# Optimization experiments

Measured on AMD Instinct MI355X. Metric: run time of the kernel, lower is better.

The kernel has to match this reference:

```python
import jax, jax.numpy as jnp
import numpy as np

N = 20000      # nodes per snapshot
E = 160000     # edges per snapshot
T = 8          # timesteps
F_IN = 256     # nfeat
HEADS = 4      # GAT heads
C = 128        # nhid_graph (per-head GAT out, concat=False -> mean)
GH = 128       # nhid_gru
NC = 2         # nclass
NEG_SLOPE = 0.2


def setup_inputs() -> dict:
    key = jax.random.key(0)
    ks = jax.random.split(key, 16)
    s = 0.05
    return {
        "graph": jax.random.randint(ks[0], (T, 2, E), 0, N),
        "fts": jax.random.normal(ks[1], (T, N, F_IN), dtype=jnp.float32),
        "time_steps": T,
        # GATConv params (PyG-style): lin weight, att_src/att_dst, bias
        "W_gat": jax.random.normal(ks[2], (F_IN, HEADS * C), dtype=jnp.float32) * s,
        "att_src": jax.random.normal(ks[3], (HEADS, C), dtype=jnp.float32) * s,
        "att_dst": jax.random.normal(ks[4], (HEADS, C), dtype=jnp.float32) * s,
        "b_gat": jax.random.normal(ks[5], (C,), dtype=jnp.float32) * s,
        # GRU params (torch layout: [3H, in], gates order r,z,n)
        "W_ih": jax.random.normal(ks[6], (3 * GH, C), dtype=jnp.float32) * s,
        "W_hh": jax.random.normal(ks[7], (3 * GH, GH), dtype=jnp.float32) * s,
        "b_ih": jax.random.normal(ks[8], (3 * GH,), dtype=jnp.float32) * s,
        "b_hh": jax.random.normal(ks[9], (3 * GH,), dtype=jnp.float32) * s,
        # Attention ('general'): linear_in [H,H] no bias, linear_out [H,2H] no bias
        "W_att_in": jax.random.normal(ks[10], (GH, GH), dtype=jnp.float32) * s,
        "W_att_out": jax.random.normal(ks[11], (GH, 2 * GH), dtype=jnp.float32) * s,
        # final classifier
        "W_cls": jax.random.normal(ks[12], (NC, GH), dtype=jnp.float32) * s,
        "b_cls": jax.random.normal(ks[13], (NC,), dtype=jnp.float32) * s,
    }


def _segment_softmax(logits, seg, num_segments):
    # logits: [E', H], seg: [E'] destination node ids
    m = jax.ops.segment_max(logits, seg, num_segments=num_segments)
    m = jnp.where(jnp.isfinite(m), m, 0.0)
    e = jnp.exp(logits - m[seg])
    s = jax.ops.segment_sum(e, seg, num_segments=num_segments)
    return e / (s[seg] + 1e-16)


def _gat_step(x, edge_index, W_gat, att_src, att_dst, b_gat):
    # PyG GATConv: concat=False (mean over heads), negative_slope=0.2,
    # add_self_loops=True; eval mode so attention dropout is identity.
    n = x.shape[0]
    xw = (x @ W_gat).reshape(n, HEADS, C)                 # [N,H,C]
    loops = jnp.arange(n, dtype=edge_index.dtype)
    src = jnp.concatenate([edge_index[0], loops])         # [E']
    dst = jnp.concatenate([edge_index[1], loops])
    a_src = jnp.einsum('nhc,hc->nh', xw, att_src)         # [N,H]
    a_dst = jnp.einsum('nhc,hc->nh', xw, att_dst)
    alpha = jax.nn.leaky_relu(a_src[src] + a_dst[dst], NEG_SLOPE)  # [E',H]
    alpha = _segment_softmax(alpha, dst, n)
    msg = xw[src] * alpha[..., None]                      # [E',H,C]
    out = jax.ops.segment_sum(msg, dst, num_segments=n)   # [N,H,C]
    return out.mean(axis=1) + b_gat                       # [N,C]


def _gru(y, W_ih, W_hh, b_ih, b_hh):
    # y: [T, N, C]; torch GRU equations, h0 = 0
    n = y.shape[1]
    def step(h, x):
        gi = x @ W_ih.T + b_ih
        gh = h @ W_hh.T + b_hh
        i_r, i_z, i_n = jnp.split(gi, 3, axis=-1)
        h_r, h_z, h_n = jnp.split(gh, 3, axis=-1)
        r = jax.nn.sigmoid(i_r + h_r)
        z = jax.nn.sigmoid(i_z + h_z)
        nn_ = jnp.tanh(i_n + r * h_n)
        h_new = (1.0 - z) * nn_ + z * h
        return h_new, h_new
    h0 = jnp.zeros((n, GH), dtype=y.dtype)
    last, full = jax.lax.scan(step, h0, y)
    return full, last  # [T,N,GH], [N,GH]


def reference(graph, fts, time_steps, W_gat, att_src, att_dst, b_gat,
              W_ih, W_hh, b_ih, b_hh, W_att_in, W_att_out, W_cls, b_cls):
    # per-timestep GAT + leaky_relu(0.2)
    ys = [jax.nn.leaky_relu(
            _gat_step(fts[i], graph[i], W_gat, att_src, att_dst, b_gat),
            NEG_SLOPE)
          for i in range(time_steps)]
    y = jnp.stack(ys)                                     # [T,N,C]
    context, last = _gru(y, W_ih, W_hh, b_ih, b_hh)
    query = last[:, None, :]                              # [N,1,GH]
    context = jnp.transpose(context, (1, 0, 2))           # [N,T,GH]
    # Attention('general')
    q = query @ W_att_in.T                                # [N,1,GH]
    scores = jnp.einsum('nod,ntd->not', q, context)       # [N,1,T]
    w = jax.nn.softmax(scores, axis=-1)
    mix = jnp.einsum('not,ntd->nod', w, context)          # [N,1,GH]
    combined = jnp.concatenate([mix, q], axis=-1)         # [N,1,2GH]
    att_out = jnp.tanh(combined @ W_att_out.T)            # [N,1,GH]
    output = jax.nn.leaky_relu(att_out.reshape(-1, GH), NEG_SLOPE)
    logits = output @ W_cls.T + b_cls                     # [N,NC]
    return jax.nn.log_softmax(logits, axis=1)
```

## Files before the change

### kernel.cpp

```cpp
#include <hip/hip_runtime.h>
#include <hip/hip_bf16.h>
#include <math.h>

#define N_NODES 20000
#define N_EDGES 160000
#define T_STEPS 8
#define F_INC   256
#define HEADS   4
#define CCH     128
#define KC      512
#define GHD     128
#define G3      384
#define SLOPE   0.2f
#define SEG     (N_EDGES + N_NODES)

typedef unsigned short u16;
typedef __attribute__((ext_vector_type(8))) short bf16x8;
typedef __attribute__((ext_vector_type(4))) float f32x4;

__device__ __forceinline__ float leakyf(float x) { return x > 0.f ? x : SLOPE * x; }
__device__ __forceinline__ float b2f(u16 u) {
  union { unsigned int i; float f; } x; x.i = ((unsigned int)u) << 16; return x.f;
}
__device__ __forceinline__ u16 f2b(float f) {
  union { float f; unsigned int i; } u; u.f = f;
  unsigned int r = u.i + 0x7FFFu + ((u.i >> 16) & 1u);
  return (u16)(r >> 16);
}
__device__ __forceinline__ float sigf(float x) { return 1.f / (1.f + expf(-x)); }

__device__ __forceinline__ void gload16(const void* g, void* l) {
  __builtin_amdgcn_global_load_lds(
      (const __attribute__((address_space(1))) unsigned int*)g,
      (__attribute__((address_space(3))) unsigned int*)l, 16, 0, 0);
}

template <int OBF, int FUSE>
__global__ __launch_bounds__(256) void gemm_bf16(
    const u16* __restrict__ A, const u16* __restrict__ B,
    const float* __restrict__ bias, void* __restrict__ Cout,
    int M, int K, int Nt, int swz,
    const float* __restrict__ attS, const float* __restrict__ attD,
    float* __restrict__ asrc, float* __restrict__ adst)
{
  __shared__ u16 As[128][32];
  __shared__ u16 Bs[128][32];
  __shared__ float s_as[128], s_ad[128];
  const int tid  = threadIdx.x;
  const int wave = tid >> 6, lane = tid & 63;
  const int wr = (wave >> 1) * 64, wc = (wave & 1) * 64;
  int bx = blockIdx.x, by = blockIdx.y;
  if (swz) {
    const int gx = gridDim.x;
    const int nwg = gx * (int)gridDim.y;
    const int lin = by * gx + bx;
    const int q = nwg >> 3, r = nwg & 7;
    const int xcd = lin & 7, idx = lin >> 3;
    const int wg = (xcd < r ? xcd * (q + 1) : r * (q + 1) + (xcd - r) * q) + idx;
    bx = wg % gx; by = wg / gx;
  }
  const int bm = by * 128, bn = bx * 128;
  const int l15 = lane & 15, g = lane >> 4;

  if (FUSE && tid < 128) { s_as[tid] = 0.f; s_ad[tid] = 0.f; }

  const int sr = tid >> 2, sd = tid & 3;
  const int ss = sd ^ ((sr >> 1) & 3);
  const u16* aS0 = A + (size_t)min(bm + sr,      M - 1) * K + ss * 8;
  const u16* aS1 = A + (size_t)min(bm + 64 + sr, M - 1) * K + ss * 8;
  const u16* bS0 = B + (size_t)(bn + sr)      * K + ss * 8;
  const u16* bS1 = B + (size_t)(bn + 64 + sr) * K + ss * 8;
  u16* lA0 = &As[0][0] + (size_t)(tid & ~63) * 8;
  u16* lA1 = lA0 + 2048;
  u16* lB0 = &Bs[0][0] + (size_t)(tid & ~63) * 8;
  u16* lB1 = lB0 + 2048;

  f32x4 acc[4][4];
  #pragma unroll
  for (int m = 0; m < 4; ++m)
    #pragma unroll
    for (int n = 0; n < 4; ++n)
      #pragma unroll
      for (int j = 0; j < 4; ++j) acc[m][n][j] = 0.f;

  const int nK = K >> 5;
  for (int kt = 0; kt < nK; ++kt) {
    const int ko = kt * 32;
    gload16(aS0 + ko, lA0);
    gload16(aS1 + ko, lA1);
    gload16(bS0 + ko, lB0);
    gload16(bS1 + ko, lB1);
    __syncthreads();
    bf16x8 af[4], bfr[4];
    #pragma unroll
    for (int m = 0; m < 4; ++m) {
      int row = wr + m * 16 + l15;
      af[m] = *(const bf16x8*)&As[row][(g ^ ((row >> 1) & 3)) * 8];
      int rowb = wc + m * 16 + l15;
      bfr[m] = *(const bf16x8*)&Bs[rowb][(g ^ ((rowb >> 1) & 3)) * 8];
    }
    #pragma unroll
    for (int m = 0; m < 4; ++m)
      #pragma unroll
      for (int n = 0; n < 4; ++n)
        acc[m][n] = __builtin_amdgcn_mfma_f32_16x16x32_bf16(af[m], bfr[n], acc[m][n], 0, 0, 0);
    __syncthreads();
  }
  #pragma unroll
  for (int m = 0; m < 4; ++m) {
    int row0 = bm + wr + m * 16 + g * 4;
    #pragma unroll
    for (int n = 0; n < 4; ++n) {
      int col = bn + wc + n * 16 + l15;
      float bv = bias ? bias[col] : 0.f;
      #pragma unroll
      for (int j = 0; j < 4; ++j) {
        int row = row0 + j;
        if (row < M) {
          float v = acc[m][n][j] + bv;
          if (OBF) ((u16*)Cout)[(size_t)row * Nt + col] = f2b(v);
          else     ((float*)Cout)[(size_t)row * Nt + col] = v;
        }
      }
    }
  }
  if (FUSE) {
    float ps[4][4], pd[4][4];
    #pragma unroll
    for (int m = 0; m < 4; ++m)
      #pragma unroll
      for (int j = 0; j < 4; ++j) { ps[m][j] = 0.f; pd[m][j] = 0.f; }
    #pragma unroll
    for (int n = 0; n < 4; ++n) {
      int cl = wc + n * 16 + l15;
      float wsv = attS[bn + cl], wdv = attD[bn + cl];
      #pragma unroll
      for (int m = 0; m < 4; ++m)
        #pragma unroll
        for (int j = 0; j < 4; ++j) {
          ps[m][j] = fmaf(acc[m][n][j], wsv, ps[m][j]);
          pd[m][j] = fmaf(acc[m][n][j], wdv, pd[m][j]);
        }
    }
    #pragma unroll
    for (int m = 0; m < 4; ++m)
      #pragma unroll
      for (int j = 0; j < 4; ++j)
        #pragma unroll
        for (int msk = 8; msk >= 1; msk >>= 1) {
          ps[m][j] += __shfl_xor(ps[m][j], msk);
          pd[m][j] += __shfl_xor(pd[m][j], msk);
        }
    if (l15 == 0) {
      #pragma unroll
      for (int m = 0; m < 4; ++m)
        #pragma unroll
        for (int j = 0; j < 4; ++j) {
          atomicAdd(&s_as[wr + m * 16 + g * 4 + j], ps[m][j]);
          atomicAdd(&s_ad[wr + m * 16 + g * 4 + j], pd[m][j]);
        }
    }
    __syncthreads();
    if (tid < 128) {
      int row = bm + tid;
      if (row < M) {
        int h = bn >> 7;
        asrc[(size_t)row * 4 + h] = s_as[tid];
        adst[(size_t)row * 4 + h] = s_ad[tid];
      }
    }
  }
}

__global__ void convert_f32_bf16(const float* __restrict__ src, u16* __restrict__ dst, int n) {
  int i = (blockIdx.x * 256 + threadIdx.x) * 8;
  if (i >= n) return;
  float4 v0 = *(const float4*)(src + i);
  float4 v1 = *(const float4*)(src + i + 4);
  bf16x8 o;
  o[0] = (short)f2b(v0.x); o[1] = (short)f2b(v0.y);
  o[2] = (short)f2b(v0.z); o[3] = (short)f2b(v0.w);
  o[4] = (short)f2b(v1.x); o[5] = (short)f2b(v1.y);
  o[6] = (short)f2b(v1.z); o[7] = (short)f2b(v1.w);
  *(bf16x8*)(dst + i) = o;
}

__global__ void convert_weights(const float* __restrict__ w_ih, const float* __restrict__ w_hh,
                                const float* __restrict__ w_in, const float* __restrict__ w_out,
                                u16* __restrict__ wihb, u16* __restrict__ whhb,
                                u16* __restrict__ winb, u16* __restrict__ woutb)
{
  int i = blockIdx.x * 256 + threadIdx.x;
  const float* src; u16* dst; int base;
  if      (i < 6144)  { src = w_ih;  dst = wihb;  base = i; }
  else if (i < 12288) { src = w_hh;  dst = whhb;  base = i - 6144; }
  else if (i < 14336) { src = w_in;  dst = winb;  base = i - 12288; }
  else                { src = w_out; dst = woutb; base = i - 14336; }
  int o = base * 8;
  float4 v0 = *(const float4*)(src + o);
  float4 v1 = *(const float4*)(src + o + 4);
  bf16x8 ov;
  ov[0] = (short)f2b(v0.x); ov[1] = (short)f2b(v0.y);
  ov[2] = (short)f2b(v0.z); ov[3] = (short)f2b(v0.w);
  ov[4] = (short)f2b(v1.x); ov[5] = (short)f2b(v1.y);
  ov[6] = (short)f2b(v1.z); ov[7] = (short)f2b(v1.w);
  *(bf16x8*)(dst + o) = ov;
}

__global__ void conv_transpose_wgat(const float* __restrict__ src, u16* __restrict__ dst) {
  int idx = blockIdx.x * 256 + threadIdx.x;
  if (idx >= KC * F_INC) return;
  int n = idx >> 8, k = idx & 255;
  dst[(size_t)n * F_INC + k] = f2b(src[(size_t)k * KC + n]);
}

__global__ void count_kernel(const int* __restrict__ graph, int* __restrict__ counts) {
  int e = blockIdx.x * 256 + threadIdx.x;
  int t = blockIdx.y;
  if (e < N_EDGES) {
    int d = graph[(size_t)t * 2 * N_EDGES + N_EDGES + e];
    atomicAdd(&counts[t * N_NODES + d], 1);
  }
}

__global__ __launch_bounds__(1024) void scan_kernel(
    const int* __restrict__ counts, int* __restrict__ offs)
{
  const int t = blockIdx.x;
  const int tid = threadIdx.x, lane = tid & 63, w = tid >> 6;
  __shared__ int s_wt[16];
  int carry = 0;
  const int base_abs = t * SEG;
  for (int base = 0; base < N_NODES; base += 1024) {
    int i = base + tid;
    int v = (i < N_NODES) ? (counts[t * N_NODES + i] + 1) : 0;
    int x = v;
    #pragma unroll
    for (int d = 1; d < 64; d <<= 1) {
      int nvl = __shfl_up(x, d, 64);
      if (lane >= d) x += nvl;
    }
    if (lane == 63) s_wt[w] = x;
    __syncthreads();
    if (tid < 16) {
      int y = s_wt[tid];
      #pragma unroll
      for (int d = 1; d < 16; d <<= 1) {
        int nvl = __shfl_up(y, d, 64);
        if (tid >= d) y += nvl;
      }
      s_wt[tid] = y;
    }
    __syncthreads();
    int wbase = (w > 0) ? s_wt[w - 1] : 0;
    int total = s_wt[15];
    if (i < N_NODES) offs[t * (N_NODES + 1) + i] = base_abs + carry + wbase + x - v;
    carry += total;
    __syncthreads();
  }
  if (tid == 0) offs[t * (N_NODES + 1) + N_NODES] = base_abs + carry;
}

__global__ void scatter_kernel(const int* __restrict__ graph, const int* __restrict__ offs,
                               int* __restrict__ cursor, int* __restrict__ ssrc)
{
  int i = blockIdx.x * 256 + threadIdx.x;
  int t = blockIdx.y;
  if (i >= SEG) return;
  int s, d;
  if (i < N_EDGES) {
    s = graph[(size_t)t * 2 * N_EDGES + i];
    d = graph[(size_t)t * 2 * N_EDGES + N_EDGES + i];
  } else {
    s = d = i - N_EDGES;
  }
  int pos = offs[t * (N_NODES + 1) + d] + atomicAdd(&cursor[t * N_NODES + d], 1);
  ssrc[pos] = s;
}

__global__ __launch_bounds__(256) void aggregate_kernel(
    const u16* __restrict__ xw, const float* __restrict__ a_src,
    const float* __restrict__ a_dst, const float* __restrict__ b_gat,
    const int* __restrict__ offs, const int* __restrict__ ssrc,
    u16* __restrict__ yout)
{
  const int wv = threadIdx.x >> 6, lane = threadIdx.x & 63;
  const int nd = blockIdx.x * 4 + wv;
  const int t  = blockIdx.y;
  __shared__ float s_w[4][64][4];
  __shared__ int   s_s[4][64];
  const int ob = t * (N_NODES + 1) + nd;
  const int beg = offs[ob], end = offs[ob + 1];
  const size_t rowbase = (size_t)t * N_NODES;
  const float4 adv = *(const float4*)&a_dst[(rowbase + nd) * 4];
  const int hl = lane >> 4;

  float m0=-INFINITY, m1=-INFINITY, m2=-INFINITY, m3=-INFINITY;
  float s0=0.f, s1=0.f, s2=0.f, s3=0.f;
  float acc[8] = {0.f,0.f,0.f,0.f,0.f,0.f,0.f,0.f};

  for (int base = beg; base < end; base += 64) {
    int e = base + lane;
    float a0=-INFINITY, a1=-INFINITY, a2=-INFINITY, a3=-INFINITY;
    if (e < end) {
      int s = ssrc[e];
      s_s[wv][lane] = s;
      float4 av = *(const float4*)&a_src[(rowbase + s) * 4];
      a0 = leakyf(av.x + adv.x); a1 = leakyf(av.y + adv.y);
      a2 = leakyf(av.z + adv.z); a3 = leakyf(av.w + adv.w);
    }
    float c0m=a0, c1m=a1, c2m=a2, c3m=a3;
    #pragma unroll
    for (int msk = 32; msk >= 1; msk >>= 1) {
      c0m = fmaxf(c0m, __shfl_xor(c0m, msk)); c1m = fmaxf(c1m, __shfl_xor(c1m, msk));
      c2m = fmaxf(c2m, __shfl_xor(c2m, msk)); c3m = fmaxf(c3m, __shfl_xor(c3m, msk));
    }
    float n0 = fmaxf(m0, c0m), n1 = fmaxf(m1, c1m), n2 = fmaxf(m2, c2m), n3 = fmaxf(m3, c3m);
    float sc0 = expf(m0 - n0), sc1 = expf(m1 - n1), sc2 = expf(m2 - n2), sc3 = expf(m3 - n3);
    float sch = (hl == 0) ? sc0 : (hl == 1) ? sc1 : (hl == 2) ? sc2 : sc3;
    #pragma unroll
    for (int k = 0; k < 8; ++k) acc[k] *= sch;
    float w0 = expf(a0 - n0), w1 = expf(a1 - n1), w2 = expf(a2 - n2), w3 = expf(a3 - n3);
    s_w[wv][lane][0] = w0; s_w[wv][lane][1] = w1;
    s_w[wv][lane][2] = w2; s_w[wv][lane][3] = w3;
    float t0=w0, t1=w1, t2=w2, t3=w3;
    #pragma unroll
    for (int msk = 32; msk >= 1; msk >>= 1) {
      t0 += __shfl_xor(t0, msk); t1 += __shfl_xor(t1, msk);
      t2 += __shfl_xor(t2, msk); t3 += __shfl_xor(t3, msk);
    }
    s0 = s0 * sc0 + t0; s1 = s1 * sc1 + t1;
    s2 = s2 * sc2 + t2; s3 = s3 * sc3 + t3;
    m0 = n0; m1 = n1; m2 = n2; m3 = n3;

    const int cnt = min(64, end - base);
#define LDX(j) (*(const int4*)&xw[(rowbase + s_s[wv][(j)]) * KC + lane * 8])
#define FMA8(W, X)                                                        \
    { float _w = (W);                                                     \
      acc[0] = fmaf(_w, __uint_as_float((unsigned)(X).x << 16), acc[0]);  \
      acc[1] = fmaf(_w, __uint_as_float((unsigned)(X).x & 0xffff0000u), acc[1]); \
      acc[2] = fmaf(_w, __uint_as_float((unsigned)(X).y << 16), acc[2]);  \
      acc[3] = fmaf(_w, __uint_as_float((unsigned)(X).y & 0xffff0000u), acc[3]); \
      acc[4] = fmaf(_w, __uint_as_float((unsigned)(X).z << 16), acc[4]);  \
      acc[5] = fmaf(_w, __uint_as_float((unsigned)(X).z & 0xffff0000u), acc[5]); \
      acc[6] = fmaf(_w, __uint_as_float((unsigned)(X).w << 16), acc[6]);  \
      acc[7] = fmaf(_w, __uint_as_float((unsigned)(X).w & 0xffff0000u), acc[7]); }
    int4 g0 = {0,0,0,0}, g1 = {0,0,0,0}, g2 = {0,0,0,0}, g3 = {0,0,0,0};
    if (0 < cnt) g0 = LDX(0);
    if (1 < cnt) g1 = LDX(1);
    if (2 < cnt) g2 = LDX(2);
    if (3 < cnt) g3 = LDX(3);
    for (int b4 = 0; b4 < cnt; b4 += 4) {
      int4 p0 = {0,0,0,0}, p1 = {0,0,0,0}, p2 = {0,0,0,0}, p3 = {0,0,0,0};
      if (b4 + 4 < cnt) p0 = LDX(b4 + 4);
      if (b4 + 5 < cnt) p1 = LDX(b4 + 5);
      if (b4 + 6 < cnt) p2 = LDX(b4 + 6);
      if (b4 + 7 < cnt) p3 = LDX(b4 + 7);
      {                      FMA8(s_w[wv][b4 + 0][hl], g0); }
      if (b4 + 1 < cnt)      { FMA8(s_w[wv][b4 + 1][hl], g1); }
      if (b4 + 2 < cnt)      { FMA8(s_w[wv][b4 + 2][hl], g2); }
      if (b4 + 3 < cnt)      { FMA8(s_w[wv][b4 + 3][hl], g3); }
      g0 = p0; g1 = p1; g2 = p2; g3 = p3;
    }
#undef LDX
#undef FMA8
  }
  float sh = (hl == 0) ? s0 : (hl == 1) ? s1 : (hl == 2) ? s2 : s3;
  float inv = 1.f / (sh + 1e-16f);
  #pragma unroll
  for (int k = 0; k < 8; ++k) {
    acc[k] *= inv;
    acc[k] += __shfl_xor(acc[k], 16);
    acc[k] += __shfl_xor(acc[k], 32);
  }
  if (lane < 16) {
    bf16x8 ov;
    #pragma unroll
    for (int k = 0; k < 8; ++k) {
      float v = acc[k] * 0.25f + b_gat[lane * 8 + k];
      ov[k] = (short)f2b(leakyf(v));
    }
    *(bf16x8*)&yout[(rowbase + nd) * GHD + lane * 8] = ov;
  }
}

__global__ void gru_combine0(const u16* __restrict__ gi_t, const float* __restrict__ b_hh,
                             u16* __restrict__ ctx0, float* __restrict__ hf)
{
  int idx = blockIdx.x * 256 + threadIdx.x;
  if (idx >= N_NODES * GHD) return;
  int n = idx >> 7, c = idx & 127;
  size_t gb = (size_t)n * G3;
  float ir = b2f(gi_t[gb + c]), iz = b2f(gi_t[gb + 128 + c]), in_ = b2f(gi_t[gb + 256 + c]);
  float r = sigf(ir + b_hh[c]);
  float z = sigf(iz + b_hh[128 + c]);
  float nn = tanhf(in_ + r * b_hh[256 + c]);
  float h = (1.f - z) * nn;
  ctx0[idx] = f2b(h);
  hf[idx] = h;
}

__global__ __launch_bounds__(256) void gru_fused(
    const u16* __restrict__ hprev, const u16* __restrict__ Whh,
    const float* __restrict__ b_hh, const u16* __restrict__ gi_t,
    float* __restrict__ hf, u16* __restrict__ ctx_out)
{
  __shared__ u16 lds[64 * 384];
  u16 (*As)[32] = (u16(*)[32])lds;
  u16 (*Bs)[32] = (u16(*)[32])(lds + 64 * 32);
  const int tid = threadIdx.x, lane = tid & 63, wv = tid >> 6;
  const int l15 = lane & 15, g = lane >> 4;
  const int bm = blockIdx.x * 64;

  const int sr = tid >> 2, sd = tid & 3;
  const int ss = sd ^ ((sr >> 1) & 3);
  const u16* aS = hprev + (size_t)min(bm + sr, N_NODES - 1) * GHD + ss * 8;
  u16* lA = lds + (size_t)(tid & ~63) * 8;
  const u16* bS[6]; u16* lB[6];
  #pragma unroll
  for (int p = 0; p < 6; ++p) {
    int r = sr + p * 64;
    bS[p] = Whh + (size_t)r * GHD + ss * 8;
    lB[p] = lds + 64 * 32 + (size_t)(p * 256 + (tid & ~63)) * 8;
  }

  f32x4 acc[4][6];
  #pragma unroll
  for (int m = 0; m < 4; ++m)
    #pragma unroll
    for (int n = 0; n < 6; ++n)
      #pragma unroll
      for (int j = 0; j < 4; ++j) acc[m][n][j] = 0.f;

  #pragma unroll
  for (int kt = 0; kt < 4; ++kt) {
    const int ko = kt * 32;
    gload16(aS + ko, lA);
    #pragma unroll
    for (int p = 0; p < 6; ++p) gload16(bS[p] + ko, lB[p]);
    __syncthreads();
    bf16x8 af[4], bfr[6];
    #pragma unroll
    for (int m = 0; m < 4; ++m) {
      int row = m * 16 + l15;
      af[m] = *(const bf16x8*)&As[row][(g ^ ((row >> 1) & 3)) * 8];
    }
    #pragma unroll
    for (int n = 0; n < 6; ++n) {
      int row = wv * 96 + n * 16 + l15;
      bfr[n] = *(const bf16x8*)&Bs[row][(g ^ ((row >> 1) & 3)) * 8];
    }
    #pragma unroll
    for (int m = 0; m < 4; ++m)
      #pragma unroll
      for (int n = 0; n < 6; ++n)
        acc[m][n] = __builtin_amdgcn_mfma_f32_16x16x32_bf16(af[m], bfr[n], acc[m][n], 0, 0, 0);
    __syncthreads();
  }
  #pragma unroll
  for (int m = 0; m < 4; ++m)
    #pragma unroll
    for (int n = 0; n < 6; ++n) {
      int c = wv * 96 + n * 16 + l15;
      float bb = b_hh[c];
      #pragma unroll
      for (int j = 0; j < 4; ++j) {
        int r = m * 16 + g * 4 + j;
        lds[r * 384 + (((c >> 3) ^ (r & 7)) << 3) + (c & 7)] = f2b(acc[m][n][j] + bb);
      }
    }
  __syncthreads();
  {
    int r = tid >> 2, gr = bm + r;
    if (gr < N_NODES) {
      const int cg = (tid & 3) * 32;
      const size_t gb = (size_t)gr * G3;
      const size_t cb = (size_t)gr * GHD;
      #pragma unroll
      for (int q = 0; q < 4; ++q) {
        int c0 = cg + q * 8;
        int sl0 = ((c0 >> 3) ^ (r & 7));
        int sl1 = (((128 + c0) >> 3) ^ (r & 7));
        int sl2 = (((256 + c0) >> 3) ^ (r & 7));
        bf16x8 hr8 = *(bf16x8*)&lds[r * 384 + sl0 * 8];
        bf16x8 hz8 = *(bf16x8*)&lds[r * 384 + sl1 * 8];
        bf16x8 hn8 = *(bf16x8*)&lds[r * 384 + sl2 * 8];
        bf16x8 ir8 = *(const bf16x8*)&gi_t[gb + c0];
        bf16x8 iz8 = *(const bf16x8*)&gi_t[gb + 128 + c0];
        bf16x8 in8 = *(const bf16x8*)&gi_t[gb + 256 + c0];
        float4 hp0 = *(const float4*)&hf[cb + c0];
        float4 hp1 = *(const float4*)&hf[cb + c0 + 4];
        float hp[8] = {hp0.x, hp0.y, hp0.z, hp0.w, hp1.x, hp1.y, hp1.z, hp1.w};
        float cv[8];
        bf16x8 hv;
        #pragma unroll
        for (int k = 0; k < 8; ++k) {
          float rr = sigf(b2f((u16)ir8[k]) + b2f((u16)hr8[k]));
          float zz = sigf(b2f((u16)iz8[k]) + b2f((u16)hz8[k]));
          float nn = tanhf(b2f((u16)in8[k]) + rr * b2f((u16)hn8[k]));
          float h = (1.f - zz) * nn + zz * hp[k];
          cv[k] = h;
          hv[k] = (short)f2b(h);
        }
        *(float4*)&hf[cb + c0]     = make_float4(cv[0], cv[1], cv[2], cv[3]);
        *(float4*)&hf[cb + c0 + 4] = make_float4(cv[4], cv[5], cv[6], cv[7]);
        *(bf16x8*)&ctx_out[cb + c0] = hv;
      }
    }
  }
}

__global__ __launch_bounds__(256) void attn_mid(
    const u16* __restrict__ ctx, const float* __restrict__ q,
    u16* __restrict__ comb)
{
  const int node = blockIdx.x * 4 + (threadIdx.x >> 6);
  const int lane = threadIdx.x & 63;
  if (node >= N_NODES) return;
  const float q0 = q[(size_t)node * GHD + lane];
  const float q1 = q[(size_t)node * GHD + 64 + lane];
  float c0[T_STEPS], c1[T_STEPS], w[T_STEPS];
  float mx = -1e30f;
  #pragma unroll
  for (int t = 0; t < T_STEPS; ++t) {
    const u16* cr = ctx + ((size_t)t * N_NODES + node) * GHD;
    c0[t] = b2f(cr[lane]); c1[t] = b2f(cr[64 + lane]);
    float p = q0 * c0[t] + q1 * c1[t];
    #pragma unroll
    for (int m = 32; m >= 1; m >>= 1) p += __shfl_xor(p, m);
    w[t] = p;
    mx = fmaxf(mx, p);
  }
  float s = 0.f;
  #pragma unroll
  for (int t = 0; t < T_STEPS; ++t) { w[t] = expf(w[t] - mx); s += w[t]; }
  const float inv = 1.f / s;
  float m0 = 0.f, m1 = 0.f;
  #pragma unroll
  for (int t = 0; t < T_STEPS; ++t) { m0 = fmaf(w[t], c0[t], m0); m1 = fmaf(w[t], c1[t], m1); }
  m0 *= inv; m1 *= inv;
  u16* cb = comb + (size_t)node * 2 * GHD;
  cb[lane]       = f2b(m0);
  cb[64 + lane]  = f2b(m1);
  cb[128 + lane] = f2b(q0);
  cb[192 + lane] = f2b(q1);
}

__global__ __launch_bounds__(256) void logits_kernel(
    const u16* __restrict__ ao, const float* __restrict__ W_cls,
    const float* __restrict__ b_cls, float* __restrict__ out)
{
  const int node = blockIdx.x * 4 + (threadIdx.x >> 6);
  const int lane = threadIdx.x & 63;
  if (node >= N_NODES) return;
  float o0 = leakyf(tanhf(b2f(ao[(size_t)node * GHD + lane])));
  float o1 = leakyf(tanhf(b2f(ao[(size_t)node * GHD + 64 + lane])));
  float p0 = o0 * W_cls[lane] + o1 * W_cls[64 + lane];
  float p1 = o0 * W_cls[128 + lane] + o1 * W_cls[192 + lane];
  #pragma unroll
  for (int m = 32; m >= 1; m >>= 1) { p0 += __shfl_xor(p0, m); p1 += __shfl_xor(p1, m); }
  if (lane == 0) {
    float l0 = p0 + b_cls[0];
    float l1 = p1 + b_cls[1];
    float mx = fmaxf(l0, l1);
    float lse = mx + logf(expf(l0 - mx) + expf(l1 - mx));
    out[(size_t)node * 2 + 0] = l0 - lse;
    out[(size_t)node * 2 + 1] = l1 - lse;
  }
}

extern "C" void kernel_launch(void* const* d_in, const int* in_sizes, int n_in,
                              void* d_out, int out_size, void* d_ws, size_t ws_size,
                              hipStream_t stream)
{
  const int*   graph     = (const int*)  d_in[0];
  const float* fts       = (const float*)d_in[1];
  const float* W_gat     = (const float*)d_in[3];
  const float* att_src   = (const float*)d_in[4];
  const float* att_dst   = (const float*)d_in[5];
  const float* b_gat     = (const float*)d_in[6];
  const float* W_ih      = (const float*)d_in[7];
  const float* W_hh      = (const float*)d_in[8];
  const float* b_ih      = (const float*)d_in[9];
  const float* b_hh      = (const float*)d_in[10];
  const float* W_att_in  = (const float*)d_in[11];
  const float* W_att_out = (const float*)d_in[12];
  const float* W_cls     = (const float*)d_in[13];
  const float* b_cls     = (const float*)d_in[14];
  float* out = (float*)d_out;

  char* ws = (char*)d_ws;
  size_t off = 0;
  auto alloc = [&](size_t bytes) {
    void* p = ws + off;
    off = (off + bytes + 255) & ~(size_t)255;
    return p;
  };
  const size_t NT = (size_t)T_STEPS * N_NODES;
  u16*   wgatT = (u16*)alloc((size_t)KC * F_INC * 2);
  u16*   wihb  = (u16*)alloc((size_t)G3 * GHD * 2);
  u16*   whhb  = (u16*)alloc((size_t)G3 * GHD * 2);
  u16*   winb  = (u16*)alloc((size_t)GHD * GHD * 2);
  u16*   woutb = (u16*)alloc((size_t)GHD * 2 * GHD * 2);
  u16*   fbf   = (u16*)alloc(NT * F_INC * 2);
  u16*   xw    = (u16*)alloc(NT * KC * 2);
  float* asrc  = (float*)alloc(NT * 4 * 4);
  float* adst  = (float*)alloc(NT * 4 * 4);
  u16*   yall  = (u16*)alloc(NT * GHD * 2);
  u16*   giall = (u16*)alloc(NT * G3 * 2);
  u16*   ctx   = (u16*)alloc(NT * GHD * 2);
  float* hf    = (float*)alloc((size_t)N_NODES * GHD * 4);
  float* qf    = (float*)alloc((size_t)N_NODES * GHD * 4);
  u16*   comb  = (u16*)alloc((size_t)N_NODES * 2 * GHD * 2);
  u16*   aob   = (u16*)alloc((size_t)N_NODES * GHD * 2);
  int* counts  = (int*)alloc((size_t)2 * T_STEPS * N_NODES * 4);
  int* cursor  = counts + T_STEPS * N_NODES;
  int* offs    = (int*)alloc((size_t)T_STEPS * (N_NODES + 1) * 4);
  int* ssrc    = (int*)alloc((size_t)T_STEPS * SEG * 4);

  conv_transpose_wgat<<<dim3((KC * F_INC + 255) / 256), 256, 0, stream>>>(W_gat, wgatT);
  convert_weights<<<dim3(72), 256, 0, stream>>>(W_ih, W_hh, W_att_in, W_att_out,
                                                wihb, whhb, winb, woutb);

  hipMemsetAsync(counts, 0, (size_t)2 * T_STEPS * N_NODES * 4, stream);
  count_kernel<<<dim3(N_EDGES / 256, T_STEPS), 256, 0, stream>>>(graph, counts);
  scan_kernel<<<dim3(T_STEPS), 1024, 0, stream>>>(counts, offs);
  scatter_kernel<<<dim3((SEG + 255) / 256, T_STEPS), 256, 0, stream>>>(graph, offs, cursor, ssrc);

  convert_f32_bf16<<<dim3((int)(NT * F_INC / 8 / 256)), 256, 0, stream>>>(
      fts, fbf, (int)(NT * F_INC));

  gemm_bf16<1, 1><<<dim3(KC / 128, (int)(NT / 128)), 256, 0, stream>>>(
      fbf, wgatT, nullptr, xw, (int)NT, F_INC, KC, 1, att_src, att_dst, asrc, adst);

  aggregate_kernel<<<dim3(N_NODES / 4, T_STEPS), 256, 0, stream>>>(
      xw, asrc, adst, b_gat, offs, ssrc, yall);

  gemm_bf16<1, 0><<<dim3(G3 / 128, (int)(NT / 128)), 256, 0, stream>>>(
      yall, wihb, b_ih, giall, (int)NT, GHD, G3, 1, nullptr, nullptr, nullptr, nullptr);

  gru_combine0<<<dim3(N_NODES * GHD / 256), 256, 0, stream>>>(giall, b_hh, ctx, hf);
  for (int t = 1; t < T_STEPS; ++t) {
    gru_fused<<<dim3((N_NODES + 63) / 64), 256, 0, stream>>>(
        ctx + (size_t)(t - 1) * N_NODES * GHD, whhb, b_hh,
        giall + (size_t)t * N_NODES * G3, hf,
        ctx + (size_t)t * N_NODES * GHD);
  }

  gemm_bf16<0, 0><<<dim3(1, (N_NODES + 127) / 128), 256, 0, stream>>>(
      ctx + (size_t)(T_STEPS - 1) * N_NODES * GHD, winb, nullptr, qf,
      N_NODES, GHD, GHD, 0, nullptr, nullptr, nullptr, nullptr);
  attn_mid<<<dim3(N_NODES / 4), 256, 0, stream>>>(ctx, qf, comb);
  gemm_bf16<1, 0><<<dim3(1, (N_NODES + 127) / 128), 256, 0, stream>>>(
      comb, woutb, nullptr, aob, N_NODES, 2 * GHD, GHD, 0, nullptr, nullptr, nullptr, nullptr);
  logits_kernel<<<dim3(N_NODES / 4), 256, 0, stream>>>(aob, W_cls, b_cls, out);
}
```

Baseline: 870.6 us.

## Restructure GAT aggregation to 16-edge chunks with lane-per-(edge,head) softmax via shuffles

The aggregate kernel now handles edges in chunks of 16, with each lane owning one (edge, head) pair. It replaces the 64-edge chunks that needed four-head reductions per lane over six shuffle stages. Source indices and attention weights move between lanes with shuffles instead of shared memory, which removes LDS traffic. Padded edges get zero weight, and the gather loop issues eight row loads at a time. With about 9 edges per node, the aim is to cut wasted lanes and reduction work, at the cost of more shuffles per edge.

```diff
diff --git a/kernel.cpp b/kernel.cpp
--- a/kernel.cpp
+++ b/kernel.cpp
@@ -287,54 +287,17 @@
   const int wv = threadIdx.x >> 6, lane = threadIdx.x & 63;
   const int nd = blockIdx.x * 4 + wv;
   const int t  = blockIdx.y;
-  __shared__ float s_w[4][64][4];
-  __shared__ int   s_s[4][64];
   const int ob = t * (N_NODES + 1) + nd;
   const int beg = offs[ob], end = offs[ob + 1];
   const size_t rowbase = (size_t)t * N_NODES;
-  const float4 adv = *(const float4*)&a_dst[(rowbase + nd) * 4];
-  const int hl = lane >> 4;
-
-  float m0=-INFINITY, m1=-INFINITY, m2=-INFINITY, m3=-INFINITY;
-  float s0=0.f, s1=0.f, s2=0.f, s3=0.f;
+  const int he   = lane & 3;
+  const int eidx = lane >> 2;
+  const int hl   = lane >> 4;
+  const float advh = a_dst[(rowbase + nd) * 4 + he];
+
+  float m = -INFINITY, ssum = 0.f;
   float acc[8] = {0.f,0.f,0.f,0.f,0.f,0.f,0.f,0.f};
 
-  for (int base = beg; base < end; base += 64) {
-    int e = base + lane;
-    float a0=-INFINITY, a1=-INFINITY, a2=-INFINITY, a3=-INFINITY;
-    if (e < end) {
-      int s = ssrc[e];
-      s_s[wv][lane] = s;
-      float4 av = *(const float4*)&a_src[(rowbase + s) * 4];
-      a0 = leakyf(av.x + adv.x); a1 = leakyf(av.y + adv.y);
-      a2 = leakyf(av.z + adv.z); a3 = leakyf(av.w + adv.w);
-    }
-    float c0m=a0, c1m=a1, c2m=a2, c3m=a3;
-    #pragma unroll
-    for (int msk = 32; msk >= 1; msk >>= 1) {
-      c0m = fmaxf(c0m, __shfl_xor(c0m, msk)); c1m = fmaxf(c1m, __shfl_xor(c1m, msk));
-      c2m = fmaxf(c2m, __shfl_xor(c2m, msk)); c3m = fmaxf(c3m, __shfl_xor(c3m, msk));
-    }
-    float n0 = fmaxf(m0, c0m), n1 = fmaxf(m1, c1m), n2 = fmaxf(m2, c2m), n3 = fmaxf(m3, c3m);
-    float sc0 = expf(m0 - n0), sc1 = expf(m1 - n1), sc2 = expf(m2 - n2), sc3 = expf(m3 - n3);
-    float sch = (hl == 0) ? sc0 : (hl == 1) ? sc1 : (hl == 2) ? sc2 : sc3;
-    #pragma unroll
-    for (int k = 0; k < 8; ++k) acc[k] *= sch;
-    float w0 = expf(a0 - n0), w1 = expf(a1 - n1), w2 = expf(a2 - n2), w3 = expf(a3 - n3);
-    s_w[wv][lane][0] = w0; s_w[wv][lane][1] = w1;
-    s_w[wv][lane][2] = w2; s_w[wv][lane][3] = w3;
-    float t0=w0, t1=w1, t2=w2, t3=w3;
-    #pragma unroll
-    for (int msk = 32; msk >= 1; msk >>= 1) {
-      t0 += __shfl_xor(t0, msk); t1 += __shfl_xor(t1, msk);
-      t2 += __shfl_xor(t2, msk); t3 += __shfl_xor(t3, msk);
-    }
-    s0 = s0 * sc0 + t0; s1 = s1 * sc1 + t1;
-    s2 = s2 * sc2 + t2; s3 = s3 * sc3 + t3;
-    m0 = n0; m1 = n1; m2 = n2; m3 = n3;
-
-    const int cnt = min(64, end - base);
-#define LDX(j) (*(const int4*)&xw[(rowbase + s_s[wv][(j)]) * KC + lane * 8])
 #define FMA8(W, X)                                                        \
     { float _w = (W);                                                     \
       acc[0] = fmaf(_w, __uint_as_float((unsigned)(X).x << 16), acc[0]);  \
@@ -345,28 +308,78 @@
       acc[5] = fmaf(_w, __uint_as_float((unsigned)(X).z & 0xffff0000u), acc[5]); \
       acc[6] = fmaf(_w, __uint_as_float((unsigned)(X).w << 16), acc[6]);  \
       acc[7] = fmaf(_w, __uint_as_float((unsigned)(X).w & 0xffff0000u), acc[7]); }
-    int4 g0 = {0,0,0,0}, g1 = {0,0,0,0}, g2 = {0,0,0,0}, g3 = {0,0,0,0};
-    if (0 < cnt) g0 = LDX(0);
-    if (1 < cnt) g1 = LDX(1);
-    if (2 < cnt) g2 = LDX(2);
-    if (3 < cnt) g3 = LDX(3);
-    for (int b4 = 0; b4 < cnt; b4 += 4) {
-      int4 p0 = {0,0,0,0}, p1 = {0,0,0,0}, p2 = {0,0,0,0}, p3 = {0,0,0,0};
-      if (b4 + 4 < cnt) p0 = LDX(b4 + 4);
-      if (b4 + 5 < cnt) p1 = LDX(b4 + 5);
-      if (b4 + 6 < cnt) p2 = LDX(b4 + 6);
-      if (b4 + 7 < cnt) p3 = LDX(b4 + 7);
-      {                      FMA8(s_w[wv][b4 + 0][hl], g0); }
-      if (b4 + 1 < cnt)      { FMA8(s_w[wv][b4 + 1][hl], g1); }
-      if (b4 + 2 < cnt)      { FMA8(s_w[wv][b4 + 2][hl], g2); }
-      if (b4 + 3 < cnt)      { FMA8(s_w[wv][b4 + 3][hl], g3); }
-      g0 = p0; g1 = p1; g2 = p2; g3 = p3;
-    }
-#undef LDX
+#define LDE(SVAR) (*(const int4*)&xw[(rowbase + (SVAR)) * KC + lane * 8])
+
+  for (int base = beg; base < end; base += 16) {
+    const int cnt = min(16, end - base);
+    const int e = base + eidx;
+    const int sidx = (e < end) ? ssrc[e] : ssrc[base];
+    const float av = a_src[(rowbase + sidx) * 4 + he];
+    const float a = (eidx < cnt) ? leakyf(av + advh) : -INFINITY;
+    float cm = a;
+    cm = fmaxf(cm, __shfl_xor(cm, 4));
+    cm = fmaxf(cm, __shfl_xor(cm, 8));
+    cm = fmaxf(cm, __shfl_xor(cm, 16));
+    cm = fmaxf(cm, __shfl_xor(cm, 32));
+    const float nm = fmaxf(m, cm);
+    const float sc = expf(m - nm);
+    const float w = expf(a - nm);
+    float ts = w;
+    ts += __shfl_xor(ts, 4);
+    ts += __shfl_xor(ts, 8);
+    ts += __shfl_xor(ts, 16);
+    ts += __shfl_xor(ts, 32);
+    ssum = ssum * sc + ts;
+    m = nm;
+    const float schl = __shfl(sc, hl);
+    #pragma unroll
+    for (int k = 0; k < 8; ++k) acc[k] *= schl;
+
+    const int cpad = (cnt + 3) & ~3;
+    int b4 = 0;
+    for (; b4 + 8 <= cpad; b4 += 8) {
+      const int s0 = __shfl(sidx, (b4 + 0) << 2);
+      const int s1 = __shfl(sidx, (b4 + 1) << 2);
+      const int s2 = __shfl(sidx, (b4 + 2) << 2);
+      const int s3 = __shfl(sidx, (b4 + 3) << 2);
+      const int s4 = __shfl(sidx, (b4 + 4) << 2);
+      const int s5 = __shfl(sidx, (b4 + 5) << 2);
+      const int s6 = __shfl(sidx, (b4 + 6) << 2);
+      const int s7 = __shfl(sidx, (b4 + 7) << 2);
+      const int4 x0 = LDE(s0); const int4 x1 = LDE(s1);
+      const int4 x2 = LDE(s2); const int4 x3 = LDE(s3);
+      const int4 x4 = LDE(s4); const int4 x5 = LDE(s5);
+      const int4 x6 = LDE(s6); const int4 x7 = LDE(s7);
+      const float w0 = __shfl(w, ((b4 + 0) << 2) + hl);
+      const float w1 = __shfl(w, ((b4 + 1) << 2) + hl);
+      const float w2 = __shfl(w, ((b4 + 2) << 2) + hl);
+      const float w3 = __shfl(w, ((b4 + 3) << 2) + hl);
+      const float w4 = __shfl(w, ((b4 + 4) << 2) + hl);
+      const float w5 = __shfl(w, ((b4 + 5) << 2) + hl);
+      const float w6 = __shfl(w, ((b4 + 6) << 2) + hl);
+      const float w7 = __shfl(w, ((b4 + 7) << 2) + hl);
+      FMA8(w0, x0); FMA8(w1, x1); FMA8(w2, x2); FMA8(w3, x3);
+      FMA8(w4, x4); FMA8(w5, x5); FMA8(w6, x6); FMA8(w7, x7);
+    }
+    if (b4 < cpad) {
+      const int s0 = __shfl(sidx, (b4 + 0) << 2);
+      const int s1 = __shfl(sidx, (b4 + 1) << 2);
+      const int s2 = __shfl(sidx, (b4 + 2) << 2);
+      const int s3 = __shfl(sidx, (b4 + 3) << 2);
+      const int4 x0 = LDE(s0); const int4 x1 = LDE(s1);
+      const int4 x2 = LDE(s2); const int4 x3 = LDE(s3);
+      const float w0 = __shfl(w, ((b4 + 0) << 2) + hl);
+      const float w1 = __shfl(w, ((b4 + 1) << 2) + hl);
+      const float w2 = __shfl(w, ((b4 + 2) << 2) + hl);
+      const float w3 = __shfl(w, ((b4 + 3) << 2) + hl);
+      FMA8(w0, x0); FMA8(w1, x1); FMA8(w2, x2); FMA8(w3, x3);
+    }
+  }
+#undef LDE
 #undef FMA8
-  }
-  float sh = (hl == 0) ? s0 : (hl == 1) ? s1 : (hl == 2) ? s2 : s3;
-  float inv = 1.f / (sh + 1e-16f);
+
+  const float sh = __shfl(ssum, hl);
+  const float inv = 1.f / (sh + 1e-16f);
   #pragma unroll
   for (int k = 0; k < 8; ++k) {
     acc[k] *= inv;
```

New measurement: 827.0 us. -5.0%, faster.
